# Kernel tuning notes

Measured on AMD Instinct MI355X. Metric: run time of the kernel, lower is better.

Reference implementation:

```python
import jax, jax.numpy as jnp
import numpy as np

N = 100000
E = 1600000
D_IN, H1, H2 = 64, 128, 64
ATT = 32


def _mean_aggregate(feat, src, dst, num_nodes):
    # gather source features per edge, scatter-sum to destinations, divide by in-degree
    summed = jax.ops.segment_sum(feat[src], dst, num_segments=num_nodes)  # [N, d]
    deg = jax.ops.segment_sum(jnp.ones((src.shape[0],), feat.dtype), dst, num_segments=num_nodes)
    return summed / jnp.maximum(deg, 1.0)[:, None]


def setup_inputs() -> dict:
    key = jax.random.key(0)
    ks = jax.random.split(key, 16)
    x = jax.random.normal(ks[0], (N, D_IN), dtype=jnp.float32)
    edge_index = jax.random.randint(ks[1], (2, E), 0, N, dtype=jnp.int64)

    def lin(k, fan_in, fan_out):
        bound = 1.0 / np.sqrt(fan_in)
        return jax.random.uniform(k, (fan_in, fan_out), jnp.float32, -bound, bound)

    params = {
        'W1_l': lin(ks[2], D_IN, H1), 'W1_r': lin(ks[3], D_IN, H1),
        'b1': jnp.zeros((H1,), jnp.float32),
        'W2_l': lin(ks[4], H1, H2), 'W2_r': lin(ks[5], H1, H2),
        'b2': jnp.zeros((H2,), jnp.float32),
        'Wa': lin(ks[6], H2, ATT), 'ba': jnp.zeros((ATT,), jnp.float32),
        'ctx': jax.random.normal(ks[7], (ATT,), jnp.float32),
        'Wc1': lin(ks[8], H2, H2 // 2), 'bc1': jnp.zeros((H2 // 2,), jnp.float32),
        'Wc2': lin(ks[9], H2 // 2, 1), 'bc2': jnp.zeros((1,), jnp.float32),
    }
    return {'x': x, 'edge_index': edge_index, **params}


def reference(x, edge_index, W1_l, W1_r, b1, W2_l, W2_r, b2, Wa, ba, ctx, Wc1, bc1, Wc2, bc2):
    src, dst = edge_index[0], edge_index[1]
    ionm_alerts = x[:, -1]  # [N]

    # GraphSAGE layer 1 (mean aggr): lin_l(mean_neighbors) + lin_r(x_self)
    agg1 = _mean_aggregate(x, src, dst, N)
    h = jax.nn.relu(agg1 @ W1_l + b1 + x @ W1_r)  # [N, H1]
    # F.dropout(training=False) -> identity

    # GraphSAGE layer 2
    agg2 = _mean_aggregate(h, src, dst, N)
    h = jax.nn.relu(agg2 @ W2_l + b2 + h @ W2_r)  # [N, H2]

    # attention with IONM alert boost (+0.4)
    scores = jnp.tanh(h @ Wa + ba)            # [N, ATT]
    w = scores @ ctx + ionm_alerts * 0.4       # [N]
    w = jax.nn.softmax(w, axis=0)
    h = h * w[:, None]

    pooled = jnp.mean(h, axis=0, keepdims=True)  # [1, H2]

    # classifier head (Dropout identity in eval)
    z = jax.nn.relu(pooled @ Wc1 + bc1)
    return jax.nn.sigmoid(z @ Wc2 + bc2)  # [1, 1]
```

## Files before the change

kernel.cpp:

```cpp
#include <hip/hip_runtime.h>
#include <math.h>

#define N_NODES 100000
#define E_EDGES 1600000
#define D_IN 64
#define HID1 128
#define HID2 64
#define ATT 32
#define CAP 32
#define AT_STRIDE 136
#define NRANGE 8
#define RNODES (N_NODES / NRANGE)
#define NPART 64
#define XCAST_BLOCKS ((N_NODES * 16 + 255) / 256)
#define NBLK 1024
#define EPB  1563
#define SEGCAP 384
#define SCAT2_BLOCKS 4096
#define GBLK 3125

#define SX 0.4f
#define INVSX 2.5f
#define SV 0.25f
#define INVSV 4.0f

typedef unsigned int uint32;
typedef unsigned short ushort;
typedef __attribute__((ext_vector_type(8))) short short8;
typedef __attribute__((ext_vector_type(4))) float float4v;
typedef __attribute__((ext_vector_type(2))) unsigned int uint32x2;

#define NTL(p) __builtin_nontemporal_load(&(p))

__device__ inline uint32 bf16rn(float f){ uint32 u = __float_as_uint(f); return (u + 0x7fffu + ((u >> 16) & 1u)) >> 16; }
__device__ inline uint32 packbf2(float a, float b){ return bf16rn(a) | (bf16rn(b) << 16); }

__device__ inline int swz3125(int bb){
    int x = bb & 7, k = bb >> 3;
    return (x < 5) ? x * 391 + k : 5 * 391 + (x - 5) * 390 + k;
}

#if __has_builtin(__builtin_amdgcn_sdot8)
#define HW_SDOT8 1
#endif

__device__ inline uint32 q4(float v, float inv){
    float n = rintf(v * inv);
    n = fminf(fmaxf(n, -8.f), 7.f);
    return (uint32)((int)n) & 15u;
}

__device__ inline void dec4i(uint32 w, int sh, int& a0, int& a1, int& a2, int& a3){
    a0 += ((int)(w << (28 - sh))) >> 28;
    a1 += ((int)(w << (24 - sh))) >> 28;
    a2 += ((int)(w << (20 - sh))) >> 28;
    a3 += ((int)(w << (16 - sh))) >> 28;
}

__global__ void k_mega(const float* __restrict__ x,
                       const int* __restrict__ src, const int* __restrict__ dst,
                       const float* __restrict__ W1l, const float* __restrict__ W1r,
                       const float* __restrict__ W2l, const float* __restrict__ W2r,
                       uint32* __restrict__ xb, uint32* __restrict__ xq4,
                       uint32* __restrict__ vq4, float* __restrict__ alertv,
                       ushort* __restrict__ wt1g, ushort* __restrict__ wt2g,
                       uint32x2* __restrict__ qu, int* __restrict__ qlen){
    int b = blockIdx.x, t = threadIdx.x;
    if (b < XCAST_BLOCKS){
        int i = b * 256 + t;
        if (i < N_NODES * 16){
            float4v v = NTL(((const float4v*)x)[i]);
            xb[2 * i]     = packbf2(v.x, v.y);
            xb[2 * i + 1] = packbf2(v.z, v.w);
            ((ushort*)xq4)[i] = (ushort)(q4(v.x, INVSX) | (q4(v.y, INVSX) << 4)
                              | (q4(v.z, INVSX) << 8) | (q4(v.w, INVSX) << 12));
            if ((i & 15) == 15) alertv[i >> 4] = v.w;
        }
        return;
    }
    if (b < XCAST_BLOCKS + 2){
        int sub = b - XCAST_BLOCKS;
        ushort* dstp = (sub == 0) ? wt1g : wt2g;
        for (int idx = t; idx < 128 * 128; idx += 256){
            int nn = idx >> 7, kk = idx & 127;
            float v;
            if (sub == 0) v = (kk < 64) ? W1l[kk * 128 + nn] : W1r[(kk - 64) * 128 + nn];
            else          v = (nn < 64) ? W2l[kk * 64 + nn]  : W2r[kk * 64 + (nn - 64)];
            dstp[nn * 128 + kk] = (ushort)bf16rn(v);
        }
        if (sub == 0){
            if (t < 8) xq4[(size_t)N_NODES * 8 + t] = 0u;
            else if (t < 16) vq4[(size_t)N_NODES * 8 + (t - 8)] = 0u;
        }
        return;
    }
    int blk = b - (XCAST_BLOCKS + 2);
    __shared__ int tails[NRANGE];
    if (t < NRANGE) tails[t] = 0;
    __syncthreads();
    int lane = t & 63;
    int base = blk * EPB;
    int end  = min(base + EPB, E_EDGES);
    for (int i0 = base; i0 < end; i0 += 256){
        int i = i0 + t;
        bool v = (i < end);
        int d = 0, s = 0, r = NRANGE;
        if (v){
            d = NTL(dst[i]);
            s = NTL(src[i]);
            r = (int)((uint32)d / (uint32)RNODES);
        }
        int mybase = 0, myoff = 0;
        #pragma unroll
        for (int k = 0; k < NRANGE; k++){
            unsigned long long mk = __ballot(r == k);
            if (r == k){
                int leader = (int)__ffsll((unsigned long long)mk) - 1;
                int nk = (int)__popcll(mk);
                int bse = 0;
                if (lane == leader) bse = atomicAdd(&tails[k], nk);
                bse = __shfl(bse, leader, 64);
                mybase = bse;
                myoff  = (int)__popcll(mk & ((lane == 63) ? 0x7fffffffffffffffull
                                                          : ((1ull << lane) - 1ull)));
            }
        }
        if (v){
            int pos = mybase + myoff;
            if (pos < SEGCAP)
                qu[(size_t)(blk * NRANGE + r) * SEGCAP + pos] = (uint32x2){(uint32)d, (uint32)s};
        }
    }
    __syncthreads();
    if (t < NRANGE) qlen[blk * NRANGE + t] = min(tails[t], SEGCAP);
}

__global__ __launch_bounds__(256) void k_scat2(const uint32x2* __restrict__ qu,
                                               const int* __restrict__ qlen,
                                               int* __restrict__ cnt, int* __restrict__ ssrc){
    int bb = blockIdx.x, t = threadIdx.x;
    int r = bb & (NRANGE - 1);
    int sidx = bb >> 3;
    #pragma unroll 1
    for (int k = 0; k < NBLK / (SCAT2_BLOCKS / NRANGE); k++){
        int seg = sidx * (NBLK / (SCAT2_BLOCKS / NRANGE)) + k;
        int qi = seg * NRANGE + r;
        int len = min(qlen[qi], SEGCAP);
        const uint32x2* qp = &qu[(size_t)qi * SEGCAP];
        for (int i = t; i < len; i += 256){
            uint32x2 pr = NTL(qp[i]);
            int d = (int)pr.x, s = (int)pr.y;
            int pos = atomicAdd(&cnt[d], 1);
            if (pos < CAP) ssrc[d * CAP + pos] = s;
        }
    }
}

__device__ inline void gather8_i4(const uint32* __restrict__ tab4,
                                  const int* __restrict__ ssrc,
                                  const int* __restrict__ cnt,
                                  int n0, int lane,
                                  int acc[8][4], int cct[8]){
    int q = lane >> 4, p = lane & 15;
    int dw = p >> 1, sh = (p & 1) << 4;
#ifdef HW_SDOT8
    uint32 sel0 = 1u << sh;
#endif
    int sr[8];
    #pragma unroll
    for (int j = 0; j < 8; j++)
        sr[j] = NTL(ssrc[(n0 + j) * CAP + lane]);
    int nn = n0 + (lane & 7);
    int ccl_ = cnt[nn];
    int cc[8];
    #pragma unroll
    for (int j = 0; j < 8; j++){
        int c = __shfl(ccl_, j, 64);
        cct[j] = c;
        cc[j] = min(c, CAP);
    }
    #pragma unroll
    for (int j = 0; j < 8; j++){ acc[j][0] = acc[j][1] = acc[j][2] = acc[j][3] = 0; }
    int cmax = 0;
    #pragma unroll
    for (int j = 0; j < 8; j++) cmax = max(cmax, cc[j]);
    if (cmax == 0) return;
    int se[8];
    #pragma unroll
    for (int j = 0; j < 8; j++)
        se[j] = (lane < cc[j]) ? sr[j] : N_NODES;

    uint32 w[4][8];
    #pragma unroll
    for (int g = 0; g < 4; g++){
        #pragma unroll
        for (int j = 0; j < 8; j++){
            int s = __shfl(se[j], g * 4 + q, 64);
            w[g][j] = tab4[(uint32)s * 8u + dw];
        }
    }
    #pragma unroll
    for (int g = 0; g < 4; g++){
        #pragma unroll
        for (int j = 0; j < 8; j++){
#ifdef HW_SDOT8
            acc[j][0] = __builtin_amdgcn_sdot8((int)w[g][j], (int)sel0,         acc[j][0], false);
            acc[j][1] = __builtin_amdgcn_sdot8((int)w[g][j], (int)(sel0 << 4),  acc[j][1], false);
            acc[j][2] = __builtin_amdgcn_sdot8((int)w[g][j], (int)(sel0 << 8),  acc[j][2], false);
            acc[j][3] = __builtin_amdgcn_sdot8((int)w[g][j], (int)(sel0 << 12), acc[j][3], false);
#else
            dec4i(w[g][j], sh, acc[j][0], acc[j][1], acc[j][2], acc[j][3]);
#endif
        }
    }
    if (cmax > 16){
        #pragma unroll
        for (int g = 0; g < 4; g++){
            #pragma unroll
            for (int j = 0; j < 8; j++){
                int s = __shfl(se[j], 16 + g * 4 + q, 64);
                w[g][j] = tab4[(uint32)s * 8u + dw];
            }
        }
        #pragma unroll
        for (int g = 0; g < 4; g++){
            #pragma unroll
            for (int j = 0; j < 8; j++){
#ifdef HW_SDOT8
                acc[j][0] = __builtin_amdgcn_sdot8((int)w[g][j], (int)sel0,         acc[j][0], false);
                acc[j][1] = __builtin_amdgcn_sdot8((int)w[g][j], (int)(sel0 << 4),  acc[j][1], false);
                acc[j][2] = __builtin_amdgcn_sdot8((int)w[g][j], (int)(sel0 << 8),  acc[j][2], false);
                acc[j][3] = __builtin_amdgcn_sdot8((int)w[g][j], (int)(sel0 << 12), acc[j][3], false);
#else
                dec4i(w[g][j], sh, acc[j][0], acc[j][1], acc[j][2], acc[j][3]);
#endif
            }
        }
    }
    #pragma unroll
    for (int j = 0; j < 8; j++){
        acc[j][0] += __shfl_xor(acc[j][0], 16, 64); acc[j][1] += __shfl_xor(acc[j][1], 16, 64);
        acc[j][2] += __shfl_xor(acc[j][2], 16, 64); acc[j][3] += __shfl_xor(acc[j][3], 16, 64);
        acc[j][0] += __shfl_xor(acc[j][0], 32, 64); acc[j][1] += __shfl_xor(acc[j][1], 32, 64);
        acc[j][2] += __shfl_xor(acc[j][2], 32, 64); acc[j][3] += __shfl_xor(acc[j][3], 32, 64);
    }
}

__device__ inline float inv_deg(int c){ return 1.f / fmaxf(fminf((float)c, (float)CAP), 1.f); }

__global__ __launch_bounds__(256) void k_layer1(
    const uint32* __restrict__ xq4, const uint32* __restrict__ xb,
    const int* __restrict__ ssrc, const int* __restrict__ cnt,
    const ushort* __restrict__ wt1g, const ushort* __restrict__ wt2g,
    const float* __restrict__ b1, const float* __restrict__ b2,
    uint32* __restrict__ vq4, ushort* __restrict__ r2b,
    float* __restrict__ pzero){
    __shared__ ushort smem[2 * 32 * AT_STRIDE];
    ushort* at  = smem;
    ushort* at2 = smem + 32 * AT_STRIDE;
    float* vstage = (float*)smem;
    int t = threadIdx.x, wave = t >> 6, lane = t & 63;
    if (blockIdx.x == 0){
        for (int i = t; i < NPART * 65; i += 256) pzero[i] = 0.f;
    }
    int nb0 = swz3125((int)blockIdx.x) * 32;
    int n0 = nb0 + wave * 8;

    int m0 = t >> 3, ch = t & 7;
    uint4 xval = *(const uint4*)&xb[(size_t)(nb0 + m0) * 32 + ch * 4];

    int acc[8][4]; int cct[8];
    gather8_i4(xq4, ssrc, cnt, n0, lane, acc, cct);
    int p = lane & 15;
    if (lane < 16){
        #pragma unroll
        for (int j = 0; j < 8; j++){
            float f = SX * inv_deg(cct[j]);
            uint2 o;
            o.x = packbf2((float)acc[j][0] * f, (float)acc[j][1] * f);
            o.y = packbf2((float)acc[j][2] * f, (float)acc[j][3] * f);
            *(uint2*)&at[(wave * 8 + j) * AT_STRIDE + 4 * p] = o;
        }
    }
    *(uint4*)((uint32*)(at + m0 * AT_STRIDE + 64) + ch * 4) = xval;
    __syncthreads();

    int cidx = lane & 15, quad = lane >> 4;
    int mt = wave >> 1;
    int nbase = (wave & 1) * 64;
    float4v c[4];
    #pragma unroll
    for (int nt = 0; nt < 4; nt++) c[nt] = (float4v){0.f,0.f,0.f,0.f};
    #pragma unroll
    for (int kt = 0; kt < 4; kt++){
        short8 a = *(short8*)(at + ((mt * 16 + cidx) * AT_STRIDE + kt * 32 + quad * 8));
        #pragma unroll
        for (int nt = 0; nt < 4; nt++){
            short8 b = *(const short8*)(wt1g + ((nbase + nt * 16 + cidx) * 128 + kt * 32 + quad * 8));
            c[nt] = __builtin_amdgcn_mfma_f32_16x16x32_bf16(a, b, c[nt], 0, 0, 0);
        }
    }
    #pragma unroll
    for (int nt = 0; nt < 4; nt++){
        float bb = b1[nbase + nt * 16 + cidx];
        #pragma unroll
        for (int i = 0; i < 4; i++){
            int row = quad * 4 + i;
            at2[(mt * 16 + row) * AT_STRIDE + nbase + nt * 16 + cidx] =
                (ushort)bf16rn(fmaxf(c[nt][i] + bb, 0.f));
        }
    }
    __syncthreads();
    #pragma unroll
    for (int nt = 0; nt < 4; nt++) c[nt] = (float4v){0.f,0.f,0.f,0.f};
    #pragma unroll
    for (int kt = 0; kt < 4; kt++){
        short8 a = *(short8*)(at2 + ((mt * 16 + cidx) * AT_STRIDE + kt * 32 + quad * 8));
        #pragma unroll
        for (int nt = 0; nt < 4; nt++){
            short8 b = *(const short8*)(wt2g + ((nbase + nt * 16 + cidx) * 128 + kt * 32 + quad * 8));
            c[nt] = __builtin_amdgcn_mfma_f32_16x16x32_bf16(a, b, c[nt], 0, 0, 0);
        }
    }
    if (nbase == 0){
        #pragma unroll
        for (int nt = 0; nt < 4; nt++){
            #pragma unroll
            for (int i = 0; i < 4; i++){
                int row = quad * 4 + i;
                vstage[(mt * 16 + row) * 65 + nt * 16 + cidx] = c[nt][i];
            }
        }
    } else {
        #pragma unroll
        for (int nt = 0; nt < 4; nt++){
            float bb = b2[nt * 16 + cidx];
            #pragma unroll
            for (int i = 0; i < 4; i++){
                int row = quad * 4 + i;
                size_t node = nb0 + mt * 16 + row;
                r2b[node * 64 + nt * 16 + cidx] = (ushort)bf16rn(c[nt][i] + bb);
            }
        }
    }
    __syncthreads();
    {
        int m = t >> 3, u = t & 7;
        float f0 = vstage[m * 65 + 8 * u],     f1 = vstage[m * 65 + 8 * u + 1];
        float f2 = vstage[m * 65 + 8 * u + 2], f3 = vstage[m * 65 + 8 * u + 3];
        float f4 = vstage[m * 65 + 8 * u + 4], f5 = vstage[m * 65 + 8 * u + 5];
        float f6 = vstage[m * 65 + 8 * u + 6], f7 = vstage[m * 65 + 8 * u + 7];
        vq4[(size_t)(nb0 + m) * 8 + u] =
              q4(f0, INVSV)        | (q4(f1, INVSV) << 4)  | (q4(f2, INVSV) << 8)
            | (q4(f3, INVSV) << 12)| (q4(f4, INVSV) << 16) | (q4(f5, INVSV) << 20)
            | (q4(f6, INVSV) << 24)| (q4(f7, INVSV) << 28);
    }
}

__device__ inline float bf16lo(uint32 u){ return __uint_as_float(u << 16); }
__device__ inline float bf16hi(uint32 u){ return __uint_as_float(u & 0xffff0000u); }

__global__ __launch_bounds__(256) void k_gather2f(
    const float* __restrict__ alertv, const uint32* __restrict__ vq4,
    const int* __restrict__ ssrc, const int* __restrict__ cnt,
    const ushort* __restrict__ r2b,
    const float* __restrict__ Wa, const float* __restrict__ ba, const float* __restrict__ ctx,
    float* __restrict__ pooledP, float* __restrict__ Zpart){
    __shared__ float sh2[32][68];
    __shared__ float sew[32];
    __shared__ float sp[4][64];
    int t = threadIdx.x, wave = t >> 6, lane = t & 63;
    int bn0 = swz3125((int)blockIdx.x) * 32;
    int n0 = bn0 + wave * 8;
    int acc[8][4]; int cct[8];
    gather8_i4(vq4, ssrc, cnt, n0, lane, acc, cct);
    int p = lane & 15;
    if (lane < 16){
        #pragma unroll
        for (int j = 0; j < 8; j++){
            size_t nj = n0 + j;
            float f = SV * inv_deg(cct[j]);
            uint32x2 rr = NTL(*(const uint32x2*)&r2b[nj * 64 + 4 * p]);
            float4v hv;
            hv.x = fmaxf((float)acc[j][0] * f + bf16lo(rr.x), 0.f);
            hv.y = fmaxf((float)acc[j][1] * f + bf16hi(rr.x), 0.f);
            hv.z = fmaxf((float)acc[j][2] * f + bf16lo(rr.y), 0.f);
            hv.w = fmaxf((float)acc[j][3] * f + bf16hi(rr.y), 0.f);
            *(float4v*)&sh2[wave * 8 + j][4 * p] = hv;
        }
    }
    __syncthreads();
    int node = t >> 3;
    int c0 = (t & 7) * 4;
    float s0 = ba[c0], s1 = ba[c0 + 1], s2 = ba[c0 + 2], s3 = ba[c0 + 3];
    #pragma unroll 8
    for (int j = 0; j < 64; j++){
        float hv = sh2[node][j];
        s0 += hv * Wa[j * ATT + c0];
        s1 += hv * Wa[j * ATT + c0 + 1];
        s2 += hv * Wa[j * ATT + c0 + 2];
        s3 += hv * Wa[j * ATT + c0 + 3];
    }
    float pa = tanhf(s0) * ctx[c0] + tanhf(s1) * ctx[c0 + 1]
             + tanhf(s2) * ctx[c0 + 2] + tanhf(s3) * ctx[c0 + 3];
    #pragma unroll
    for (int off = 4; off >= 1; off >>= 1) pa += __shfl_down(pa, off, 8);
    if ((t & 7) == 0){
        int n = bn0 + node;
        float w = pa + NTL(alertv[n]) * 0.4f;
        sew[node] = expf(w);
    }
    __syncthreads();
    int j = t & 63, q = t >> 6;
    float p4 = 0.f;
    #pragma unroll
    for (int m = 0; m < 8; m++) p4 += sh2[q * 8 + m][j] * sew[q * 8 + m];
    sp[q][j] = p4;
    __syncthreads();
    if (t < 64){
        float s = sp[0][t] + sp[1][t] + sp[2][t] + sp[3][t];
        atomicAdd(&pooledP[(blockIdx.x & (NPART - 1)) * 64 + t], s);
    }
    if (t == 64){
        float z = 0.f;
        #pragma unroll
        for (int m = 0; m < 32; m++) z += sew[m];
        atomicAdd(&Zpart[blockIdx.x & (NPART - 1)], z);
    }
}

__global__ void k_final(const float* __restrict__ pooledP, const float* __restrict__ Zpart,
                        const float* __restrict__ Wc1, const float* __restrict__ bc1,
                        const float* __restrict__ Wc2, const float* __restrict__ bc2,
                        float* __restrict__ out){
    __shared__ float sp[64], sz[32];
    __shared__ float Zs;
    int t = threadIdx.x;
    float s = 0.f;
    for (int q = 0; q < NPART; q++) s += pooledP[q * 64 + t];
    if (t == 0){
        float z = 0.f;
        for (int q = 0; q < NPART; q++) z += Zpart[q];
        Zs = z;
    }
    __syncthreads();
    float scale = 1.0f / (Zs * (float)N_NODES);
    sp[t] = s * scale;
    __syncthreads();
    if (t < 32){
        float a = bc1[t];
        #pragma unroll 8
        for (int j = 0; j < 64; j++) a += sp[j] * Wc1[j * 32 + t];
        sz[t] = fmaxf(a, 0.f);
    }
    __syncthreads();
    if (t == 0){
        float a = bc2[0];
        #pragma unroll
        for (int i = 0; i < 32; i++) a += sz[i] * Wc2[i];
        out[0] = 1.0f / (1.0f + expf(-a));
    }
}

extern "C" void kernel_launch(void* const* d_in, const int* in_sizes, int n_in,
                              void* d_out, int out_size, void* d_ws, size_t ws_size,
                              hipStream_t stream) {
    const float* x   = (const float*)d_in[0];
    const int*   ei  = (const int*)d_in[1];
    const int*   src = ei;
    const int*   dst = ei + E_EDGES;
    const float* W1l = (const float*)d_in[2];
    const float* W1r = (const float*)d_in[3];
    const float* b1  = (const float*)d_in[4];
    const float* W2l = (const float*)d_in[5];
    const float* W2r = (const float*)d_in[6];
    const float* b2  = (const float*)d_in[7];
    const float* Wa  = (const float*)d_in[8];
    const float* ba  = (const float*)d_in[9];
    const float* ctx = (const float*)d_in[10];
    const float* Wc1 = (const float*)d_in[11];
    const float* bc1 = (const float*)d_in[12];
    const float* Wc2 = (const float*)d_in[13];
    const float* bc2 = (const float*)d_in[14];

    char* p = (char*)d_ws;
    int* cnt    = (int*)p;                 p += (size_t)N_NODES * 4;
    int* ssrc   = (int*)p;                 p += (size_t)N_NODES * CAP * 4;
    uint32* xb  = (uint32*)p;              p += (size_t)N_NODES * 32 * 4;
    uint32* xq4 = (uint32*)p;              p += (size_t)(N_NODES + 1) * 8 * 4;
    uint32* vq4 = (uint32*)p;              p += (size_t)(N_NODES + 1) * 8 * 4;
    char* r2region = p;                    p += (size_t)N_NODES * 64 * 4;
    ushort* wt1g = (ushort*)p;             p += 128 * 128 * 2;
    ushort* wt2g = (ushort*)p;             p += 128 * 128 * 2;
    float* pooledP = (float*)p;            p += NPART * 64 * 4;
    float* Zpart   = (float*)p;            p += NPART * 4;
    int* qlen      = (int*)p;              p += (size_t)NBLK * NRANGE * 4;
    float* alertv  = (float*)p;            p += (size_t)N_NODES * 4;
    uint32x2* qu = (uint32x2*)r2region;
    ushort* r2b  = (ushort*)r2region;

    hipMemsetAsync(cnt, 0, (size_t)N_NODES * 4, stream);

    k_mega<<<XCAST_BLOCKS + 2 + NBLK, 256, 0, stream>>>(
        x, src, dst, W1l, W1r, W2l, W2r, xb, xq4, vq4, alertv, wt1g, wt2g, qu, qlen);

    k_scat2<<<SCAT2_BLOCKS, 256, 0, stream>>>(qu, qlen, cnt, ssrc);

    k_layer1<<<GBLK, 256, 0, stream>>>(xq4, xb, ssrc, cnt,
                                       wt1g, wt2g, b1, b2, vq4, r2b, pooledP);
    k_gather2f<<<GBLK, 256, 0, stream>>>(alertv, vq4, ssrc, cnt, r2b,
                                         Wa, ba, ctx, pooledP, Zpart);
    k_final<<<1, 64, 0, stream>>>(pooledP, Zpart, Wc1, bc1, Wc2, bc2, (float*)d_out);
}
```

Measured before the change: 308.3 us.

## Interleave x-cast blocks with edge scatter kernel and fold cnt memset

Moves the x bf16/int4 conversion out of the edge-binning kernel into the scatter kernel, interleaving cast blocks with scatter blocks so the latency-bound atomic scatter overlaps with the bandwidth-bound cast. The separate memset of the degree counters is replaced by zeroing inside the binning kernel. This removes one launch and rebalances work between the two kernels. The risk is that the interleaving adds contention, and the xq4 padding writes in block 0 of k_mega still depend on the cast happening elsewhere.

Result: no change. 306.9 us, median of 2 (-0.5%).

```diff
diff --git a/kernel.cpp b/kernel.cpp
--- a/kernel.cpp
+++ b/kernel.cpp
@@ -17,6 +17,8 @@
 #define EPB  1563
 #define SEGCAP 384
 #define SCAT2_BLOCKS 4096
+#define ILV (2 * SCAT2_BLOCKS)
+#define SCX_BLOCKS (ILV + XCAST_BLOCKS - SCAT2_BLOCKS)
 #define GBLK 3125
 
 #define SX 0.4f
@@ -57,29 +59,16 @@
     a3 += ((int)(w << (16 - sh))) >> 28;
 }
 
-__global__ void k_mega(const float* __restrict__ x,
-                       const int* __restrict__ src, const int* __restrict__ dst,
+__global__ void k_mega(const int* __restrict__ src, const int* __restrict__ dst,
                        const float* __restrict__ W1l, const float* __restrict__ W1r,
                        const float* __restrict__ W2l, const float* __restrict__ W2r,
-                       uint32* __restrict__ xb, uint32* __restrict__ xq4,
-                       uint32* __restrict__ vq4, float* __restrict__ alertv,
+                       uint32* __restrict__ xq4, uint32* __restrict__ vq4,
                        ushort* __restrict__ wt1g, ushort* __restrict__ wt2g,
-                       uint32x2* __restrict__ qu, int* __restrict__ qlen){
+                       uint32x2* __restrict__ qu, int* __restrict__ qlen,
+                       int* __restrict__ cnt){
     int b = blockIdx.x, t = threadIdx.x;
-    if (b < XCAST_BLOCKS){
-        int i = b * 256 + t;
-        if (i < N_NODES * 16){
-            float4v v = NTL(((const float4v*)x)[i]);
-            xb[2 * i]     = packbf2(v.x, v.y);
-            xb[2 * i + 1] = packbf2(v.z, v.w);
-            ((ushort*)xq4)[i] = (ushort)(q4(v.x, INVSX) | (q4(v.y, INVSX) << 4)
-                              | (q4(v.z, INVSX) << 8) | (q4(v.w, INVSX) << 12));
-            if ((i & 15) == 15) alertv[i >> 4] = v.w;
-        }
-        return;
-    }
-    if (b < XCAST_BLOCKS + 2){
-        int sub = b - XCAST_BLOCKS;
+    if (b < 2){
+        int sub = b;
         ushort* dstp = (sub == 0) ? wt1g : wt2g;
         for (int idx = t; idx < 128 * 128; idx += 256){
             int nn = idx >> 7, kk = idx & 127;
@@ -94,7 +83,8 @@
         }
         return;
     }
-    int blk = b - (XCAST_BLOCKS + 2);
+    int blk = b - 2;
+    for (int i = blk * 256 + t; i < N_NODES; i += NBLK * 256) cnt[i] = 0;
     __shared__ int tails[NRANGE];
     if (t < NRANGE) tails[t] = 0;
     __syncthreads();
@@ -135,23 +125,40 @@
     if (t < NRANGE) qlen[blk * NRANGE + t] = min(tails[t], SEGCAP);
 }
 
-__global__ __launch_bounds__(256) void k_scat2(const uint32x2* __restrict__ qu,
-                                               const int* __restrict__ qlen,
-                                               int* __restrict__ cnt, int* __restrict__ ssrc){
-    int bb = blockIdx.x, t = threadIdx.x;
-    int r = bb & (NRANGE - 1);
-    int sidx = bb >> 3;
-    #pragma unroll 1
-    for (int k = 0; k < NBLK / (SCAT2_BLOCKS / NRANGE); k++){
-        int seg = sidx * (NBLK / (SCAT2_BLOCKS / NRANGE)) + k;
-        int qi = seg * NRANGE + r;
-        int len = min(qlen[qi], SEGCAP);
-        const uint32x2* qp = &qu[(size_t)qi * SEGCAP];
-        for (int i = t; i < len; i += 256){
-            uint32x2 pr = NTL(qp[i]);
-            int d = (int)pr.x, s = (int)pr.y;
-            int pos = atomicAdd(&cnt[d], 1);
-            if (pos < CAP) ssrc[d * CAP + pos] = s;
+__global__ __launch_bounds__(256) void k_scx(
+    const uint32x2* __restrict__ qu, const int* __restrict__ qlen,
+    int* __restrict__ cnt, int* __restrict__ ssrc,
+    const float* __restrict__ x, uint32* __restrict__ xb,
+    uint32* __restrict__ xq4, float* __restrict__ alertv){
+    int b = blockIdx.x, t = threadIdx.x;
+    int role, idx;
+    if (b < ILV){ role = b & 1; idx = b >> 1; }
+    else        { role = 1;     idx = b - ILV + SCAT2_BLOCKS; }
+    if (role == 0){
+        int r = idx & (NRANGE - 1);
+        int sidx = idx >> 3;
+        #pragma unroll 1
+        for (int k = 0; k < NBLK / (SCAT2_BLOCKS / NRANGE); k++){
+            int seg = sidx * (NBLK / (SCAT2_BLOCKS / NRANGE)) + k;
+            int qi = seg * NRANGE + r;
+            int len = min(qlen[qi], SEGCAP);
+            const uint32x2* qp = &qu[(size_t)qi * SEGCAP];
+            for (int i = t; i < len; i += 256){
+                uint32x2 pr = NTL(qp[i]);
+                int d = (int)pr.x, s = (int)pr.y;
+                int pos = atomicAdd(&cnt[d], 1);
+                if (pos < CAP) ssrc[d * CAP + pos] = s;
+            }
+        }
+    } else {
+        int i = idx * 256 + t;
+        if (i < N_NODES * 16){
+            float4v v = NTL(((const float4v*)x)[i]);
+            xb[2 * i]     = packbf2(v.x, v.y);
+            xb[2 * i + 1] = packbf2(v.z, v.w);
+            ((ushort*)xq4)[i] = (ushort)(q4(v.x, INVSX) | (q4(v.y, INVSX) << 4)
+                              | (q4(v.z, INVSX) << 8) | (q4(v.w, INVSX) << 12));
+            if ((i & 15) == 15) alertv[i >> 4] = v.w;
         }
     }
 }
@@ -499,12 +506,10 @@
     uint32x2* qu = (uint32x2*)r2region;
     ushort* r2b  = (ushort*)r2region;
 
-    hipMemsetAsync(cnt, 0, (size_t)N_NODES * 4, stream);
-
-    k_mega<<<XCAST_BLOCKS + 2 + NBLK, 256, 0, stream>>>(
-        x, src, dst, W1l, W1r, W2l, W2r, xb, xq4, vq4, alertv, wt1g, wt2g, qu, qlen);
-
-    k_scat2<<<SCAT2_BLOCKS, 256, 0, stream>>>(qu, qlen, cnt, ssrc);
+    k_mega<<<2 + NBLK, 256, 0, stream>>>(
+        src, dst, W1l, W1r, W2l, W2r, xq4, vq4, wt1g, wt2g, qu, qlen, cnt);
+
+    k_scx<<<SCX_BLOCKS, 256, 0, stream>>>(qu, qlen, cnt, ssrc, x, xb, xq4, alertv);
 
     k_layer1<<<GBLK, 256, 0, stream>>>(xq4, xb, ssrc, cnt,
                                        wt1g, wt2g, b1, b2, vq4, r2b, pooledP);
```
